# Optimization experiments

Hardware: AMD Instinct MI355X
Metric: run time of the kernel (lower is better)

Reference implementation:

```python
import jax, jax.numpy as jnp
import numpy as np

NH = 1024
VS = 50257
CUT0 = 1675          # round(VS/30)
CUT1 = 3 * CUT0      # 5025
N_CLUSTERS = 2
HEAD_SIZE = CUT0 + N_CLUSTERS          # 1677
D0, D1 = NH // 4, NH // 16             # 256, 64
SZ0, SZ1 = CUT1 - CUT0, VS - CUT1      # 3350, 45232


def setup_inputs() -> dict:
    key = jax.random.key(0)
    ks = jax.random.split(key, 8)
    s = 0.02
    return {
        "x": jax.random.normal(ks[0], (8, 512, NH), dtype=jnp.float32),
        "y": jax.random.randint(ks[1], (8, 512), 0, VS, dtype=jnp.int64),
        "head_w": jax.random.normal(ks[2], (HEAD_SIZE, NH), dtype=jnp.float32) * s,
        "head_b": jnp.zeros((HEAD_SIZE,), dtype=jnp.float32),
        "proj0": jax.random.normal(ks[3], (D0, NH), dtype=jnp.float32) * s,
        "w0": jax.random.normal(ks[4], (SZ0, D0), dtype=jnp.float32) * s,
        "proj1": jax.random.normal(ks[5], (D1, NH), dtype=jnp.float32) * s,
        "w1": jax.random.normal(ks[6], (SZ1, D1), dtype=jnp.float32) * s,
    }


def reference(x, y, head_w, head_b, proj0, w0, proj1, w1):
    # Flatten as in the torch forward: x -> [N, nh], y -> [N]
    xf = x.reshape(-1, x.shape[-1])            # [N, NH]
    yf = y.reshape(-1)                         # [N]

    # Head: shortlist tokens + 2 cluster logits
    head_logits = jnp.einsum('nh,vh->nv', xf, head_w) + head_b   # [N, 1677]
    head_lp = jax.nn.log_softmax(head_logits, axis=-1)

    # Default: target in head shortlist
    in_head = yf < CUT0
    idx_head = jnp.where(in_head, yf, 0)
    out = jnp.take_along_axis(head_lp, idx_head[:, None], axis=1)[:, 0]

    # Tail clusters: dense per-cluster small GEMMs + log-softmax, masked select
    for i, (low, high, proj, w) in enumerate(
            [(CUT0, CUT1, proj0, w0), (CUT1, VS, proj1, w1)]):
        size = high - low
        h = jnp.einsum('nh,dh->nd', xf, proj)          # [N, d_i]
        lp = jax.nn.log_softmax(jnp.einsum('nd,vd->nv', h, w), axis=-1)  # [N, size]
        rel = jnp.clip(yf - low, 0, size - 1)
        cl = head_lp[:, CUT0 + i] + jnp.take_along_axis(lp, rel[:, None], axis=1)[:, 0]
        mask = (yf >= low) & (yf < high)
        out = jnp.where(mask, cl, out)

    loss = -jnp.mean(out)
    return out, loss
```

## Files before the change

### kernel.cpp

```cpp
#include <hip/hip_runtime.h>
#include <stdint.h>

#define NROWS 4096
#define NHID 1024
#define CC0 1675
#define CC1 5025
#define HEADSZ 1677
#define PD0 256
#define PD1 64
#define TSZ0 3350
#define TSZ1 45232
#define HPN (HEADSZ + PD0 + PD1)
#define TPC1 6
#define L2E 1.4426950408889634f
#define LN2 0.6931471805599453f

#define NB_C0 864
#define NB_C1 1888
#define NB_TG 1024
#define NB_TAIL (NB_C0 + NB_C1 + NB_TG)

typedef __attribute__((ext_vector_type(8))) __bf16 bf16x8;
typedef __attribute__((ext_vector_type(4))) float f32x4;

__device__ __forceinline__ unsigned short f2bf(float f) {
  union { float f; uint32_t u; } v; v.f = f;
  return (unsigned short)((v.u + 0x7FFFu + ((v.u >> 16) & 1u)) >> 16);
}
__device__ __forceinline__ float bfl(uint32_t u) {
  union { uint32_t u; float f; } v; v.u = u << 16; return v.f;
}
__device__ __forceinline__ float bfh(uint32_t u) {
  union { uint32_t u; float f; } v; v.u = u & 0xFFFF0000u; return v.f;
}
__device__ __forceinline__ float bf1(unsigned short u) {
  union { uint32_t u; float f; } v; v.u = ((uint32_t)u) << 16; return v.f;
}
#define EXP2(x) __builtin_amdgcn_exp2f(x)

#define CV1 1048576
#define CV2 1477888
#define CV3 1543424
#define CV4 1559808
#define CV5 1774208
#define CV6 2497920
__global__ void conv_all(const float* __restrict__ x, const float* __restrict__ hw,
                         const float* __restrict__ p0, const float* __restrict__ p1,
                         const float* __restrict__ w0, const float* __restrict__ w1,
                         unsigned short* __restrict__ dst) {
  int stride = gridDim.x * blockDim.x;
  for (int i = blockIdx.x * blockDim.x + threadIdx.x; i < CV6; i += stride) {
    const float* src; int off; float sc;
    if (i < CV1)      { src = x;  off = i;       sc = 1.f; }
    else if (i < CV2) { src = hw; off = i - CV1; sc = L2E; }
    else if (i < CV3) { src = p0; off = i - CV2; sc = 1.f; }
    else if (i < CV4) { src = p1; off = i - CV3; sc = 1.f; }
    else if (i < CV5) { src = w0; off = i - CV4; sc = L2E; }
    else              { src = w1; off = i - CV5; sc = L2E; }
    float4 v = reinterpret_cast<const float4*>(src)[off];
    ushort4 o;
    o.x = f2bf(v.x * sc); o.y = f2bf(v.y * sc);
    o.z = f2bf(v.z * sc); o.w = f2bf(v.w * sc);
    reinterpret_cast<ushort4*>(dst)[i] = o;
  }
}

#define GLOAD(g, l) __builtin_amdgcn_global_load_lds( \
    (const __attribute__((address_space(1))) uint32_t*)(const void*)(g), \
    (__attribute__((address_space(3))) uint32_t*)(void*)(l), 16, 0, 0)

#define SWZB(L) ((L) ^ ((((L) >> 7) & 7) << 4))

__device__ __forceinline__
void gemm_core(const unsigned short* __restrict__ A, int lda,
               const unsigned short* __restrict__ B, int ldb,
               int N, int K, int tile0, int tile1, int brow,
               const float* __restrict__ bias,
               float* __restrict__ sum_out,
               unsigned short* __restrict__ Cout, int ldc, int coutStart,
               unsigned short* AsB, unsigned short* BsB) {
  const int tid = threadIdx.x;
  const int lane = tid & 63;
  const int wid = tid >> 6;
  const int wrow = (wid >> 1) * 64;
  const int wcol = (wid & 1) * 64;
  const int lr = lane & 15, lg = lane >> 4;
  const int nsteps = (tile1 - tile0) * (K >> 5);
  const int rowBase = brow + wrow;

  float sacc[4][4];
#pragma unroll
  for (int m = 0; m < 4; ++m)
#pragma unroll
    for (int r = 0; r < 4; ++r) sacc[m][r] = 0.f;

  auto stage = [&](int b, int tt, int kk) {
#pragma unroll
    for (int c = 0; c < 2; ++c) {
      int g = wid * 128 + c * 64 + lane;
      int L = g * 16;
      int S = SWZB(L);
      int row = S >> 6, ko = (S >> 4) & 3;
      GLOAD(A + (size_t)(brow + row) * lda + kk + ko * 8, (char*)AsB + b * 8192 + L);
      int bsrc = tt * 128 + row; bsrc = bsrc < N ? bsrc : N - 1;
      GLOAD(B + (size_t)bsrc * ldb + kk + ko * 8, (char*)BsB + b * 8192 + L);
    }
  };

  f32x4 acc[4][4];
#pragma unroll
  for (int m = 0; m < 4; ++m)
#pragma unroll
    for (int n = 0; n < 4; ++n) acc[m][n] = (f32x4){0.f, 0.f, 0.f, 0.f};

  int tp = tile0, kp = 0;
  auto adv = [&](int& t, int& k) { k += 32; if (k == K) { k = 0; ++t; } };
  stage(0, tp, kp); adv(tp, kp);
  if (nsteps > 1) { stage(1, tp, kp); adv(tp, kp); }

  int tile = tile0, k0 = 0;
  for (int s = 0; s < nsteps; ++s) {
    if (s + 1 < nsteps) asm volatile("s_waitcnt vmcnt(4)" ::: "memory");
    else                asm volatile("s_waitcnt vmcnt(0)" ::: "memory");
    __builtin_amdgcn_s_barrier();
    if (s + 2 < nsteps) { stage((s + 2) % 3, tp, kp); adv(tp, kp); }

    const int cur = s % 3;
    int k0n = k0 + 32, tn = tile;
    if (k0n == K) { k0n = 0; tn = tile + 1; }

    bf16x8 af[4], bfv[4];
#pragma unroll
    for (int m = 0; m < 4; ++m)
      af[m] = *(const bf16x8*)((const char*)AsB + cur * 8192 +
                               SWZB((wrow + m * 16 + lr) * 64 + lg * 16));
#pragma unroll
    for (int n = 0; n < 4; ++n)
      bfv[n] = *(const bf16x8*)((const char*)BsB + cur * 8192 +
                                SWZB((wcol + n * 16 + lr) * 64 + lg * 16));
#pragma unroll
    for (int m = 0; m < 4; ++m)
#pragma unroll
      for (int n = 0; n < 4; ++n)
        acc[m][n] = __builtin_amdgcn_mfma_f32_16x16x32_bf16(af[m], bfv[n], acc[m][n], 0, 0, 0);

    if (tn != tile) {
      const int cb = tile * 128 + wcol;
#pragma unroll
      for (int m = 0; m < 4; ++m)
#pragma unroll
        for (int n = 0; n < 4; ++n) {
#pragma unroll
          for (int r = 0; r < 4; ++r) {
            int col = cb + n * 16 + lr;
            if (col < N) {
              float v = acc[m][n][r];
              if (Cout && col >= coutStart) {
                int row = rowBase + m * 16 + lg * 4 + r;
                Cout[(size_t)row * ldc + (col - coutStart)] = f2bf(v);
              } else {
                if (bias) v = fmaf(bias[col], L2E, v);
                sacc[m][r] += EXP2(v);
              }
            }
          }
          acc[m][n] = (f32x4){0.f, 0.f, 0.f, 0.f};
        }
    }
    tile = tn; k0 = k0n;
  }

#pragma unroll
  for (int m = 0; m < 4; ++m)
#pragma unroll
    for (int r = 0; r < 4; ++r) {
      float s = sacc[m][r];
      s += __shfl_xor(s, 1); s += __shfl_xor(s, 2);
      s += __shfl_xor(s, 4); s += __shfl_xor(s, 8);
      if (lr == 0) atomicAdd(&sum_out[rowBase + m * 16 + lg * 4 + r], s);
    }
}

__global__ __launch_bounds__(256, 2)
void gemm_head(const unsigned short* __restrict__ A,
               const unsigned short* __restrict__ B,
               const float* __restrict__ bias,
               float* __restrict__ sum_out,
               unsigned short* __restrict__ Cout) {
  __shared__ __align__(16) unsigned short As[3 * 4096];
  __shared__ __align__(16) unsigned short Bs[3 * 4096];
  const int cpx = 512 >> 3;
  const int sid = ((int)blockIdx.x & 7) * cpx + ((int)blockIdx.x >> 3);
  const int rowBlk = sid & 31;
  const int colChunk = sid >> 5;
  gemm_core(A, NHID, B, NHID, HPN, NHID, colChunk, colChunk + 1, rowBlk * 128,
            bias, sum_out, Cout, PD0 + PD1, HEADSZ, As, Bs);
}

__global__ __launch_bounds__(256, 3)
void fused_tail(const unsigned short* __restrict__ hb,
                const unsigned short* __restrict__ w0b,
                const unsigned short* __restrict__ w1b,
                const unsigned short* __restrict__ xb,
                const unsigned short* __restrict__ hwb,
                const float* __restrict__ head_b,
                const int* __restrict__ y,
                float* __restrict__ s0, float* __restrict__ s1,
                float* __restrict__ ht, float* __restrict__ tc) {
  __shared__ __align__(16) unsigned short lds[6 * 4096];
  const int bid = blockIdx.x;

  if (bid < NB_C0) {
    const int cpx = NB_C0 >> 3;
    const int sid = (bid & 7) * cpx + (bid >> 3);
    const int rowBlk = sid & 31;
    const int colChunk = sid >> 5;
    gemm_core(hb, PD0 + PD1, w0b, PD0, TSZ0, PD0, colChunk, colChunk + 1,
              rowBlk * 128, nullptr, s0, nullptr, 0, 0, lds, lds + 3 * 4096);
    return;
  }

  if (bid < NB_C0 + NB_C1) {
    const int b1 = bid - NB_C0;
    const int tid = threadIdx.x;
    const int lane = tid & 63;
    const int wid = tid >> 6;
    const int lr = lane & 15, lg = lane >> 4;
    const int cpx = NB_C1 >> 3;
    const int sid = (b1 & 7) * cpx + (b1 >> 3);
    const int rowBlk = sid & 31;
    const int colChunk = sid >> 5;
    const int rowBase = rowBlk * 128 + (wid >> 1) * 64;
    const int wcol = (wid & 1) * 64;
    const int tile0 = colChunk * TPC1;

    int colOff[4], srcOff[4];
#pragma unroll
    for (int c = 0; c < 4; ++c) {
      int L = (c * 256 + tid) * 16;
      int S = L ^ (((L >> 7) & 7) << 4);
      colOff[c] = S >> 7;
      srcOff[c] = (S & 127) >> 1;
    }
    auto stage = [&](int b, int t) {
#pragma unroll
      for (int c = 0; c < 4; ++c) {
        int gc = t * 128 + colOff[c];
        gc = gc < TSZ1 ? gc : TSZ1 - 1;
        GLOAD(w1b + (size_t)gc * PD1 + srcOff[c],
              (char*)lds + b * 16384 + (c * 256 + tid) * 16);
      }
    };

    bf16x8 af[4][2];
#pragma unroll
    for (int m = 0; m < 4; ++m) {
      const unsigned short* p = hb + PD0 +
          (size_t)(rowBase + m * 16 + lr) * (PD0 + PD1) + lg * 8;
      af[m][0] = *(const bf16x8*)p;
      af[m][1] = *(const bf16x8*)(p + 32);
    }

    float sacc[4][4];
#pragma unroll
    for (int m = 0; m < 4; ++m)
#pragma unroll
      for (int r = 0; r < 4; ++r) sacc[m][r] = 0.f;

    stage(0, tile0);
    stage(1, tile0 + 1);

#pragma unroll 1
    for (int s = 0; s < TPC1; ++s) {
      if (s + 1 < TPC1) asm volatile("s_waitcnt vmcnt(4)" ::: "memory");
      else              asm volatile("s_waitcnt vmcnt(0)" ::: "memory");
      __builtin_amdgcn_s_barrier();
      if (s + 2 < TPC1) stage((s + 2) % 3, tile0 + s + 2);

      const int cur = s % 3;
      const int cb = (tile0 + s) * 128 + wcol;
      const int full = (cb + 63 < TSZ1);

#pragma unroll
      for (int nh = 0; nh < 2; ++nh) {
        bf16x8 bf[2][2];
#pragma unroll
        for (int nn = 0; nn < 2; ++nn) {
          int ccol = wcol + (nh * 2 + nn) * 16 + lr;
#pragma unroll
          for (int kh = 0; kh < 2; ++kh) {
            int L = ccol * 128 + kh * 64 + lg * 16;
            bf[nn][kh] = *(const bf16x8*)((const char*)lds + cur * 16384 +
                                          (L ^ ((ccol & 7) << 4)));
          }
        }
        f32x4 acc[4][2];
#pragma unroll
        for (int m = 0; m < 4; ++m)
#pragma unroll
          for (int nn = 0; nn < 2; ++nn) {
            f32x4 a = (f32x4){0.f, 0.f, 0.f, 0.f};
            a = __builtin_amdgcn_mfma_f32_16x16x32_bf16(af[m][0], bf[nn][0], a, 0, 0, 0);
            a = __builtin_amdgcn_mfma_f32_16x16x32_bf16(af[m][1], bf[nn][1], a, 0, 0, 0);
            acc[m][nn] = a;
          }
        if (full) {
#pragma unroll
          for (int m = 0; m < 4; ++m)
#pragma unroll
            for (int r = 0; r < 4; ++r)
              sacc[m][r] += EXP2(acc[m][0][r]) + EXP2(acc[m][1][r]);
        } else {
#pragma unroll
          for (int m = 0; m < 4; ++m)
#pragma unroll
            for (int r = 0; r < 4; ++r) {
              float t = 0.f;
#pragma unroll
              for (int nn = 0; nn < 2; ++nn)
                if (cb + (nh * 2 + nn) * 16 + lr < TSZ1) t += EXP2(acc[m][nn][r]);
              sacc[m][r] += t;
            }
        }
      }
    }

#pragma unroll
    for (int m = 0; m < 4; ++m)
#pragma unroll
      for (int r = 0; r < 4; ++r) {
        float s = sacc[m][r];
        s += __shfl_xor(s, 1); s += __shfl_xor(s, 2);
        s += __shfl_xor(s, 4); s += __shfl_xor(s, 8);
        if (lr == 0) atomicAdd(&s1[rowBase + m * 16 + lg * 4 + r], s);
      }
    return;
  }

  {
    const int b2 = bid - NB_C0 - NB_C1;
    int row = b2 * 4 + (threadIdx.x >> 6);
    int lane = threadIdx.x & 63;
    int yv = y[row];
    int th = yv < CC0 ? yv : (yv < CC1 ? CC0 : CC0 + 1);

    const unsigned short* xr = xb + (size_t)row * NHID + lane * 16;
    const unsigned short* wr = hwb + (size_t)th * NHID + lane * 16;
    uint4 xa = *(const uint4*)xr,       wa = *(const uint4*)wr;
    uint4 xc = *(const uint4*)(xr + 8), wc = *(const uint4*)(wr + 8);
    float s = 0.f;
    uint32_t xs[8] = {xa.x, xa.y, xa.z, xa.w, xc.x, xc.y, xc.z, xc.w};
    uint32_t ws[8] = {wa.x, wa.y, wa.z, wa.w, wc.x, wc.y, wc.z, wc.w};
#pragma unroll
    for (int j = 0; j < 8; ++j)
      s += bfl(xs[j]) * bfl(ws[j]) + bfh(xs[j]) * bfh(ws[j]);
#pragma unroll
    for (int d = 1; d < 64; d <<= 1) s += __shfl_xor(s, d);

    float cl = 0.f;
    if (yv >= CC0) {
      if (yv < CC1) {
        int rel = yv - CC0;
        const unsigned short* hr = hb + (size_t)row * (PD0 + PD1) + lane * 4;
        const unsigned short* w0r = w0b + (size_t)rel * PD0 + lane * 4;
        uint2 ha = *(const uint2*)hr, wa0 = *(const uint2*)w0r;
        cl = bfl(ha.x) * bfl(wa0.x) + bfh(ha.x) * bfh(wa0.x)
           + bfl(ha.y) * bfl(wa0.y) + bfh(ha.y) * bfh(wa0.y);
      } else {
        int rel = yv - CC1;
        cl = bf1(hb[(size_t)row * (PD0 + PD1) + PD0 + lane])
           * bf1(w1b[(size_t)rel * PD1 + lane]);
      }
#pragma unroll
      for (int d = 1; d < 64; d <<= 1) cl += __shfl_xor(cl, d);
    }
    if (lane == 0) { ht[row] = s * LN2 + head_b[th]; tc[row] = (yv < CC0) ? 0.f : cl; }
  }
}

__global__ void rowloss(const float* __restrict__ hs, const float* __restrict__ ht,
                        const float* __restrict__ s0, const float* __restrict__ s1,
                        const float* __restrict__ tc,
                        const int* __restrict__ y, float* __restrict__ out) {
  int n = blockIdx.x * 256 + threadIdx.x;
  int yv = y[n];
  float o = ht[n] - __builtin_amdgcn_logf(hs[n]) * LN2;
  if (yv >= CC0)
    o += tc[n] * LN2 - __builtin_amdgcn_logf(yv < CC1 ? s0[n] : s1[n]) * LN2;
  out[n] = o;
  float l = o;
#pragma unroll
  for (int d = 1; d < 64; d <<= 1) l += __shfl_xor(l, d);
  __shared__ float red[4];
  if ((threadIdx.x & 63) == 0) red[threadIdx.x >> 6] = l;
  __syncthreads();
  if (threadIdx.x == 0)
    atomicAdd(&out[NROWS], -(red[0] + red[1] + red[2] + red[3]) / (float)NROWS);
}

extern "C" void kernel_launch(void* const* d_in, const int* in_sizes, int n_in,
                              void* d_out, int out_size, void* d_ws, size_t ws_size,
                              hipStream_t stream) {
  const float* x      = (const float*)d_in[0];
  const int*   y      = (const int*)d_in[1];
  const float* head_w = (const float*)d_in[2];
  const float* head_b = (const float*)d_in[3];
  const float* proj0  = (const float*)d_in[4];
  const float* w0     = (const float*)d_in[5];
  const float* proj1  = (const float*)d_in[6];
  const float* w1     = (const float*)d_in[7];
  float* out = (float*)d_out;

  char* wp = (char*)d_ws;
  unsigned short* xb  = (unsigned short*)wp; wp += (size_t)NROWS * NHID * 2;
  unsigned short* hpb = (unsigned short*)wp; wp += (size_t)HPN * NHID * 2;
  unsigned short* w0b = (unsigned short*)wp; wp += (size_t)TSZ0 * PD0 * 2;
  unsigned short* w1b = (unsigned short*)wp; wp += (size_t)TSZ1 * PD1 * 2;
  unsigned short* hb  = (unsigned short*)wp; wp += (size_t)NROWS * (PD0 + PD1) * 2;
  float* hs = (float*)wp; wp += NROWS * 4;
  float* s0 = (float*)wp; wp += NROWS * 4;
  float* s1 = (float*)wp; wp += NROWS * 4;
  float* ht = (float*)wp; wp += NROWS * 4;
  float* tc = (float*)wp; wp += NROWS * 4;

  hipMemsetAsync(hs, 0, 3 * NROWS * 4, stream);
  hipMemsetAsync(out + NROWS, 0, 4, stream);

  conv_all<<<dim3(2048), 256, 0, stream>>>(x, head_w, proj0, proj1, w0, w1, xb);

  gemm_head<<<dim3(512), 256, 0, stream>>>(xb, hpb, head_b, hs, hb);

  fused_tail<<<dim3(NB_TAIL), 256, 0, stream>>>(
      hb, w0b, w1b, xb, hpb, head_b, y, s0, s1, ht, tc);

  rowloss<<<dim3(NROWS / 256), 256, 0, stream>>>(hs, ht, s0, s1, tc, y, out);
}
```

Baseline: 107.2 us.

## Split head GEMM from projection GEMM and fuse head into tail kernel

The projection GEMM (x times proj0/proj1) now runs alone in a small 96-block launch, and the head logits GEMM with its exp-sum moves into the fused tail kernel as extra blocks. Previously the 512-block head+projection launch had to finish before any tail work could start. Now the head-sum work can run alongside the cluster GEMMs and the gather blocks. The cost is that the small projection launch underfills the device, and the head GEMM now runs at the fused kernel's occupancy and register budget rather than its own.

```diff
diff --git a/kernel.cpp b/kernel.cpp
--- a/kernel.cpp
+++ b/kernel.cpp
@@ -15,10 +15,11 @@
 #define L2E 1.4426950408889634f
 #define LN2 0.6931471805599453f
 
+#define NB_HD 448
 #define NB_C0 864
 #define NB_C1 1888
 #define NB_TG 1024
-#define NB_TAIL (NB_C0 + NB_C1 + NB_TG)
+#define NB_ALL (NB_HD + NB_C0 + NB_C1 + NB_TG)
 
 typedef __attribute__((ext_vector_type(8))) __bf16 bf16x8;
 typedef __attribute__((ext_vector_type(4))) float f32x4;
@@ -182,37 +183,48 @@
 }
 
 __global__ __launch_bounds__(256, 2)
-void gemm_head(const unsigned short* __restrict__ A,
+void proj_gemm(const unsigned short* __restrict__ A,
                const unsigned short* __restrict__ B,
-               const float* __restrict__ bias,
-               float* __restrict__ sum_out,
-               unsigned short* __restrict__ Cout) {
+               unsigned short* __restrict__ hb,
+               float* __restrict__ dm) {
   __shared__ __align__(16) unsigned short As[3 * 4096];
   __shared__ __align__(16) unsigned short Bs[3 * 4096];
-  const int cpx = 512 >> 3;
+  const int cpx = 96 >> 3;
   const int sid = ((int)blockIdx.x & 7) * cpx + ((int)blockIdx.x >> 3);
   const int rowBlk = sid & 31;
   const int colChunk = sid >> 5;
-  gemm_core(A, NHID, B, NHID, HPN, NHID, colChunk, colChunk + 1, rowBlk * 128,
-            bias, sum_out, Cout, PD0 + PD1, HEADSZ, As, Bs);
+  gemm_core(A, NHID, B, NHID, PD0 + PD1, NHID, colChunk, colChunk + 1,
+            rowBlk * 128, nullptr, dm, hb, PD0 + PD1, 0, As, Bs);
 }
 
 __global__ __launch_bounds__(256, 3)
-void fused_tail(const unsigned short* __restrict__ hb,
-                const unsigned short* __restrict__ w0b,
-                const unsigned short* __restrict__ w1b,
-                const unsigned short* __restrict__ xb,
-                const unsigned short* __restrict__ hwb,
-                const float* __restrict__ head_b,
-                const int* __restrict__ y,
-                float* __restrict__ s0, float* __restrict__ s1,
-                float* __restrict__ ht, float* __restrict__ tc) {
+void fused_all(const unsigned short* __restrict__ hb,
+               const unsigned short* __restrict__ w0b,
+               const unsigned short* __restrict__ w1b,
+               const unsigned short* __restrict__ xb,
+               const unsigned short* __restrict__ hwb,
+               const float* __restrict__ head_b,
+               const int* __restrict__ y,
+               float* __restrict__ hs,
+               float* __restrict__ s0, float* __restrict__ s1,
+               float* __restrict__ ht, float* __restrict__ tc) {
   __shared__ __align__(16) unsigned short lds[6 * 4096];
   const int bid = blockIdx.x;
 
-  if (bid < NB_C0) {
+  if (bid < NB_HD) {
+    const int cpx = NB_HD >> 3;
+    const int sid = (bid & 7) * cpx + (bid >> 3);
+    const int rowBlk = sid & 31;
+    const int colChunk = sid >> 5;
+    gemm_core(xb, NHID, hwb, NHID, HEADSZ, NHID, colChunk, colChunk + 1,
+              rowBlk * 128, head_b, hs, nullptr, 0, 0, lds, lds + 3 * 4096);
+    return;
+  }
+
+  if (bid < NB_HD + NB_C0) {
+    const int b0 = bid - NB_HD;
     const int cpx = NB_C0 >> 3;
-    const int sid = (bid & 7) * cpx + (bid >> 3);
+    const int sid = (b0 & 7) * cpx + (b0 >> 3);
     const int rowBlk = sid & 31;
     const int colChunk = sid >> 5;
     gemm_core(hb, PD0 + PD1, w0b, PD0, TSZ0, PD0, colChunk, colChunk + 1,
@@ -220,8 +232,8 @@
     return;
   }
 
-  if (bid < NB_C0 + NB_C1) {
-    const int b1 = bid - NB_C0;
+  if (bid < NB_HD + NB_C0 + NB_C1) {
+    const int b1 = bid - NB_HD - NB_C0;
     const int tid = threadIdx.x;
     const int lane = tid & 63;
     const int wid = tid >> 6;
@@ -338,7 +350,7 @@
   }
 
   {
-    const int b2 = bid - NB_C0 - NB_C1;
+    const int b2 = bid - NB_HD - NB_C0 - NB_C1;
     int row = b2 * 4 + (threadIdx.x >> 6);
     int lane = threadIdx.x & 63;
     int yv = y[row];
@@ -422,16 +434,18 @@
   float* s1 = (float*)wp; wp += NROWS * 4;
   float* ht = (float*)wp; wp += NROWS * 4;
   float* tc = (float*)wp; wp += NROWS * 4;
+  float* dm = (float*)wp; wp += NROWS * 4;
 
   hipMemsetAsync(hs, 0, 3 * NROWS * 4, stream);
   hipMemsetAsync(out + NROWS, 0, 4, stream);
 
   conv_all<<<dim3(2048), 256, 0, stream>>>(x, head_w, proj0, proj1, w0, w1, xb);
 
-  gemm_head<<<dim3(512), 256, 0, stream>>>(xb, hpb, head_b, hs, hb);
-
-  fused_tail<<<dim3(NB_TAIL), 256, 0, stream>>>(
-      hb, w0b, w1b, xb, hpb, head_b, y, s0, s1, ht, tc);
+  proj_gemm<<<dim3(96), 256, 0, stream>>>(
+      xb, hpb + (size_t)HEADSZ * NHID, hb, dm);
+
+  fused_all<<<dim3(NB_ALL), 256, 0, stream>>>(
+      hb, w0b, w1b, xb, hpb, head_b, y, hs, s0, s1, ht, tc);
 
   rowloss<<<dim3(NROWS / 256), 256, 0, stream>>>(hs, ht, s0, s1, tc, y, out);
 }
```

Measured after the change: 119.5 us. 1.11x slower.

## Overlap tail weight conversion with head GEMM in a fused mid kernel

Applied to the files above, without the earlier changes.

Splits the conversion kernel so only x, head weights and projections are converted first. The tail weights w0/w1 are converted inside a new fused kernel whose other blocks run the head GEMM and the projection GEMM, so the conversion overlaps with compute. The head and projection column ranges now go to separate block groups with their own tile mappings, and the projection sums go to a dummy buffer. This costs an extra block-role branch and shared LDS sizing, and the conversion blocks compete with the GEMM blocks for bandwidth.

```diff
diff --git a/kernel.cpp b/kernel.cpp
--- a/kernel.cpp
+++ b/kernel.cpp
@@ -15,6 +15,11 @@
 #define L2E 1.4426950408889634f
 #define LN2 0.6931471805599453f
 
+#define NB_HD 448
+#define NB_PJ 96
+#define NB_CW 512
+#define NB_MID (NB_HD + NB_PJ + NB_CW)
+
 #define NB_C0 864
 #define NB_C1 1888
 #define NB_TG 1024
@@ -44,19 +49,19 @@
 #define CV4 1559808
 #define CV5 1774208
 #define CV6 2497920
-__global__ void conv_all(const float* __restrict__ x, const float* __restrict__ hw,
-                         const float* __restrict__ p0, const float* __restrict__ p1,
-                         const float* __restrict__ w0, const float* __restrict__ w1,
-                         unsigned short* __restrict__ dst) {
+#define CVW0 (CV5 - CV4)
+#define CVW  (CV6 - CV4)
+
+__global__ void conv_part(const float* __restrict__ x, const float* __restrict__ hw,
+                          const float* __restrict__ p0, const float* __restrict__ p1,
+                          unsigned short* __restrict__ dst) {
   int stride = gridDim.x * blockDim.x;
-  for (int i = blockIdx.x * blockDim.x + threadIdx.x; i < CV6; i += stride) {
+  for (int i = blockIdx.x * blockDim.x + threadIdx.x; i < CV4; i += stride) {
     const float* src; int off; float sc;
     if (i < CV1)      { src = x;  off = i;       sc = 1.f; }
     else if (i < CV2) { src = hw; off = i - CV1; sc = L2E; }
     else if (i < CV3) { src = p0; off = i - CV2; sc = 1.f; }
-    else if (i < CV4) { src = p1; off = i - CV3; sc = 1.f; }
-    else if (i < CV5) { src = w0; off = i - CV4; sc = L2E; }
-    else              { src = w1; off = i - CV5; sc = L2E; }
+    else              { src = p1; off = i - CV3; sc = 1.f; }
     float4 v = reinterpret_cast<const float4*>(src)[off];
     ushort4 o;
     o.x = f2bf(v.x * sc); o.y = f2bf(v.y * sc);
@@ -181,20 +186,54 @@
     }
 }
 
-__global__ __launch_bounds__(256, 2)
-void gemm_head(const unsigned short* __restrict__ A,
-               const unsigned short* __restrict__ B,
-               const float* __restrict__ bias,
-               float* __restrict__ sum_out,
-               unsigned short* __restrict__ Cout) {
-  __shared__ __align__(16) unsigned short As[3 * 4096];
-  __shared__ __align__(16) unsigned short Bs[3 * 4096];
-  const int cpx = 512 >> 3;
-  const int sid = ((int)blockIdx.x & 7) * cpx + ((int)blockIdx.x >> 3);
-  const int rowBlk = sid & 31;
-  const int colChunk = sid >> 5;
-  gemm_core(A, NHID, B, NHID, HPN, NHID, colChunk, colChunk + 1, rowBlk * 128,
-            bias, sum_out, Cout, PD0 + PD1, HEADSZ, As, Bs);
+__global__ __launch_bounds__(256, 3)
+void fused_mid(const unsigned short* __restrict__ xb,
+               const unsigned short* __restrict__ hpb,
+               const float* __restrict__ head_b,
+               float* __restrict__ hs,
+               unsigned short* __restrict__ hb,
+               float* __restrict__ dm,
+               const float* __restrict__ w0f, const float* __restrict__ w1f,
+               unsigned short* __restrict__ dstAll) {
+  __shared__ __align__(16) unsigned short lds[6 * 4096];
+  const int bid = blockIdx.x;
+
+  if (bid < NB_HD) {
+    const int xcd = bid & 7;
+    const int local = bid >> 3;
+    const int rowBlk = xcd * 4 + local / 14;
+    const int colChunk = local % 14;
+    gemm_core(xb, NHID, hpb, NHID, HEADSZ, NHID, colChunk, colChunk + 1,
+              rowBlk * 128, head_b, hs, nullptr, 0, 0, lds, lds + 3 * 4096);
+    return;
+  }
+
+  if (bid < NB_HD + NB_PJ) {
+    const int b1 = bid - NB_HD;
+    const int cpx = NB_PJ >> 3;
+    const int sid = (b1 & 7) * cpx + (b1 >> 3);
+    const int rowBlk = sid & 31;
+    const int colChunk = sid >> 5;
+    gemm_core(xb, NHID, hpb + (size_t)HEADSZ * NHID, NHID, PD0 + PD1, NHID,
+              colChunk, colChunk + 1, rowBlk * 128,
+              nullptr, dm, hb, PD0 + PD1, 0, lds, lds + 3 * 4096);
+    return;
+  }
+
+  {
+    const int b2 = bid - NB_HD - NB_PJ;
+    const int stride = NB_CW * 256;
+    for (int i = b2 * 256 + (int)threadIdx.x; i < CVW; i += stride) {
+      const float* src; int off;
+      if (i < CVW0) { src = w0f; off = i; }
+      else          { src = w1f; off = i - CVW0; }
+      float4 v = reinterpret_cast<const float4*>(src)[off];
+      ushort4 o;
+      o.x = f2bf(v.x * L2E); o.y = f2bf(v.y * L2E);
+      o.z = f2bf(v.z * L2E); o.w = f2bf(v.w * L2E);
+      reinterpret_cast<ushort4*>(dstAll)[CV4 + i] = o;
+    }
+  }
 }
 
 __global__ __launch_bounds__(256, 3)
@@ -422,13 +461,15 @@
   float* s1 = (float*)wp; wp += NROWS * 4;
   float* ht = (float*)wp; wp += NROWS * 4;
   float* tc = (float*)wp; wp += NROWS * 4;
+  float* dm = (float*)wp; wp += NROWS * 4;
 
   hipMemsetAsync(hs, 0, 3 * NROWS * 4, stream);
   hipMemsetAsync(out + NROWS, 0, 4, stream);
 
-  conv_all<<<dim3(2048), 256, 0, stream>>>(x, head_w, proj0, proj1, w0, w1, xb);
-
-  gemm_head<<<dim3(512), 256, 0, stream>>>(xb, hpb, head_b, hs, hb);
+  conv_part<<<dim3(1024), 256, 0, stream>>>(x, head_w, proj0, proj1, xb);
+
+  fused_mid<<<dim3(NB_MID), 256, 0, stream>>>(
+      xb, hpb, head_b, hs, hb, dm, w0, w1, xb);
 
   fused_tail<<<dim3(NB_TAIL), 256, 0, stream>>>(
       hb, w0b, w1b, xb, hpb, head_b, y, s0, s1, ht, tc);
```

New measurement: 104.9 us. 2.2% less time.
